# Kernel optimization log

Hardware: AMD Instinct MI355X
Metric: run time of the kernel (lower is better)

Reference implementation:

```python
import jax, jax.numpy as jnp
import numpy as np

B, N, D, H = 4, 4096, 1024, 16
DK = D // H


def setup_inputs() -> dict:
    key = jax.random.key(0)
    ks = jax.random.split(key, 11)
    s = 0.02  # small init scale for weights
    return {
        "query": jax.random.normal(ks[0], (B, N, D), jnp.float32),
        "key": jax.random.normal(ks[1], (B, N, D), jnp.float32),
        "value": jax.random.normal(ks[2], (B, N, D), jnp.float32),
        "Wq": jax.random.normal(ks[3], (D, D), jnp.float32) * s,
        "bq": jax.random.normal(ks[4], (D,), jnp.float32) * s,
        "Wk": jax.random.normal(ks[5], (D, D), jnp.float32) * s,
        "bk": jax.random.normal(ks[6], (D,), jnp.float32) * s,
        "Wv": jax.random.normal(ks[7], (D, D), jnp.float32) * s,
        "bv": jax.random.normal(ks[8], (D,), jnp.float32) * s,
        "Wo": jax.random.normal(ks[9], (D, D), jnp.float32) * s,
        "bo": jax.random.normal(ks[10], (D,), jnp.float32) * s,
    }


def reference(query, key, value, Wq, bq, Wk, bk, Wv, bv, Wo, bo):
    b, n, d = query.shape
    h, dk = H, d // H

    def proj(x, W, bias):
        # torch Linear: y = x @ W.T + b ; then split heads -> [b,h,n,dk]
        y = x @ W.T + bias
        return y.reshape(b, n, h, dk).transpose(0, 2, 1, 3)

    q = proj(query, Wq, bq)
    k = proj(key, Wk, bk)
    v = proj(value, Wv, bv)

    # linear attention (Efficient Attention, arXiv:1812.01243)
    q = jax.nn.softmax(q, axis=-1) * (1.0 / np.sqrt(dk).astype(np.float32))
    k = jax.nn.softmax(k, axis=-2)  # softmax over sequence dim
    ctx = jnp.einsum('bhnd,bhne->bhde', k, v)   # [b,h,dk,dk]
    out = jnp.einsum('bhnd,bhde->bhne', q, ctx)  # [b,h,n,dk]

    out = out.transpose(0, 2, 1, 3).reshape(b, n, d)
    return out @ Wo.T + bo
```

## Files before the change

kernel.cpp:

```cpp
#include <hip/hip_runtime.h>
#include <hip/hip_bf16.h>

#define B_ 4
#define N_ 4096
#define D_ 1024
#define H_ 16

typedef __attribute__((ext_vector_type(4))) float f32x4;
typedef __attribute__((ext_vector_type(8))) short s16x8;

__device__ __forceinline__ ushort f2bf(float f) {
  union { float f; unsigned u; } v; v.f = f;
  unsigned u = v.u;
  return (ushort)((u + 0x7fffu + ((u >> 16) & 1u)) >> 16);
}

__device__ __forceinline__ void gld16(const ushort* g, ushort* lds_base) {
  __builtin_amdgcn_global_load_lds(
      (const __attribute__((address_space(1))) unsigned int*)g,
      (__attribute__((address_space(3))) unsigned int*)lds_base, 16, 0, 0);
}

__device__ __forceinline__ unsigned cvtpk(float lo, float hi) {
  unsigned r;
  asm("v_cvt_pk_bf16_f32 %0, %1, %2" : "=v"(r) : "v"(lo), "v"(hi));
  return r;
}

__global__ void conv_w_kernel(const float* __restrict__ w0, const float* __restrict__ w1,
                              const float* __restrict__ w2, const float* __restrict__ w3,
                              ushort* __restrict__ dst) {
  const int z = blockIdx.z;
  const float* src = z == 0 ? w0 : z == 1 ? w1 : z == 2 ? w2 : w3;
  ushort* d = dst + (long)z * (D_ * D_);
  const long i0 = ((long)blockIdx.x * 256 + threadIdx.x) * 8;
  const long STR = (long)128 * 256 * 8;
#pragma unroll
  for (int u = 0; u < 4; ++u) {
    f32x4 a = *(const f32x4*)(src + i0 + u * STR);
    f32x4 b = *(const f32x4*)(src + i0 + u * STR + 4);
    s16x8 o;
    o[0] = (short)f2bf(a[0]); o[1] = (short)f2bf(a[1]); o[2] = (short)f2bf(a[2]); o[3] = (short)f2bf(a[3]);
    o[4] = (short)f2bf(b[0]); o[5] = (short)f2bf(b[1]); o[6] = (short)f2bf(b[2]); o[7] = (short)f2bf(b[3]);
    *(s16x8*)(d + i0 + u * STR) = o;
  }
}

template <int EPI, bool AFP32>
__global__ __launch_bounds__(256, 2) void gemm_bt_kernel(
    const void* __restrict__ Av, const ushort* __restrict__ Bm,
    void* __restrict__ Cv, const float* __restrict__ bias, float* __restrict__ kpart,
    int MT, int K, long sA, long sB, long sC) {
  __shared__ ushort As[128 * 32];
  __shared__ ushort Bs[128 * 32];
  const int z = blockIdx.z;
  Bm += (long)z * sB;
  const int lin = blockIdx.x;
  const int xcd = lin & 7, idx = lin >> 3;
  const int mpx = MT >> 3;
  const int m0 = (xcd * mpx + (idx >> 3)) * 128;
  const int n0 = (idx & 7) * 128;
  const int N = 1024;
  const int tid = threadIdx.x;
  const int wave = tid >> 6, lane = tid & 63;
  const int fl = lane & 15, fh = lane >> 4;
  const int wm = wave >> 1, wn = wave & 1;
  f32x4 acc[4][4] = {};
  const int rb0 = tid >> 2, kb0 = (tid & 3) * 8;
  const int rb1 = (tid + 256) >> 2, kb1 = ((tid + 256) & 3) * 8;
  ushort* ldsB0 = Bs + wave * 512;
  ushort* ldsB1 = Bs + 2048 + wave * 512;
  ushort* ldsA0 = As + wave * 512;
  ushort* ldsA1 = As + 2048 + wave * 512;

  const float* Af = (const float*)Av;
  const ushort* Ab = (const ushort*)Av + (long)z * sA;
  const float* ap = AFP32 ? (Af + (long)(m0 + (tid >> 3)) * K + (tid & 7) * 4) : nullptr;
  ushort* wp = As + (tid >> 3) * 32 + (tid & 7) * 4;
  f32x4 areg[4];
  if constexpr (AFP32) {
#pragma unroll
    for (int u = 0; u < 4; ++u) areg[u] = *(const f32x4*)(ap + u * 32 * 1024);
  }

  for (int kk = 0; kk < K; kk += 32) {
    __syncthreads();
    gld16(Bm + (long)(n0 + rb0) * K + kk + kb0, ldsB0);
    gld16(Bm + (long)(n0 + rb1) * K + kk + kb1, ldsB1);
    if constexpr (AFP32) {
#pragma unroll
      for (int u = 0; u < 4; ++u) {
        uint2 w;
        w.x = cvtpk(areg[u][0], areg[u][1]);
        w.y = cvtpk(areg[u][2], areg[u][3]);
        *(uint2*)(wp + u * 1024) = w;
      }
      if (kk + 32 < K) {
#pragma unroll
        for (int u = 0; u < 4; ++u)
          areg[u] = *(const f32x4*)(ap + u * 32 * 1024 + kk + 32);
      }
    } else {
      gld16(Ab + (long)(m0 + rb0) * K + kk + kb0, ldsA0);
      gld16(Ab + (long)(m0 + rb1) * K + kk + kb1, ldsA1);
    }
    __syncthreads();
    s16x8 fa[4], fb[4];
#pragma unroll
    for (int i = 0; i < 4; ++i)
      fa[i] = *(const s16x8*)(As + (wm * 64 + i * 16 + fl) * 32 + fh * 8);
#pragma unroll
    for (int j = 0; j < 4; ++j)
      fb[j] = *(const s16x8*)(Bs + (wn * 64 + j * 16 + fl) * 32 + fh * 8);
#pragma unroll
    for (int i = 0; i < 4; ++i)
#pragma unroll
      for (int j = 0; j < 4; ++j)
        acc[i][j] = __builtin_amdgcn_mfma_f32_16x16x32_bf16(fa[i], fb[j], acc[i][j], 0, 0, 0);
  }

  if constexpr (EPI == 0) {
    ushort* C = (ushort*)Cv;
#pragma unroll
    for (int j = 0; j < 4; ++j) {
      int col = n0 + wn * 64 + j * 16 + fl;
#pragma unroll
      for (int i = 0; i < 4; ++i)
#pragma unroll
        for (int r = 0; r < 4; ++r) {
          int row = m0 + wm * 64 + i * 16 + fh * 4 + r;
          C[(long)row * N + col] = f2bf(acc[i][j][r]);
        }
    }
  } else if constexpr (EPI == 1) {
    ushort* C = (ushort*)Cv;
    float bcol[4];
#pragma unroll
    for (int j = 0; j < 4; ++j) bcol[j] = bias[n0 + wn * 64 + j * 16 + fl];
#pragma unroll
    for (int i = 0; i < 4; ++i)
#pragma unroll
      for (int r = 0; r < 4; ++r) {
        float v[4];
#pragma unroll
        for (int j = 0; j < 4; ++j) v[j] = acc[i][j][r] + bcol[j];
        float m = fmaxf(fmaxf(v[0], v[1]), fmaxf(v[2], v[3]));
#pragma unroll
        for (int o = 1; o <= 8; o <<= 1) m = fmaxf(m, __shfl_xor(m, o));
        float e[4], s = 0.f;
#pragma unroll
        for (int j = 0; j < 4; ++j) { e[j] = __expf(v[j] - m); s += e[j]; }
#pragma unroll
        for (int o = 1; o <= 8; o <<= 1) s += __shfl_xor(s, o);
        float sc = 0.125f / s;
        int row = m0 + wm * 64 + i * 16 + fh * 4 + r;
#pragma unroll
        for (int j = 0; j < 4; ++j)
          C[(long)row * N + n0 + wn * 64 + j * 16 + fl] = f2bf(e[j] * sc);
      }
  } else if constexpr (EPI == 2) {
    ushort* C = (ushort*)Cv;
    float csum[4] = {};
#pragma unroll
    for (int j = 0; j < 4; ++j) {
      int col = n0 + wn * 64 + j * 16 + fl;
#pragma unroll
      for (int i = 0; i < 4; ++i)
#pragma unroll
        for (int r = 0; r < 4; ++r) {
          int row = m0 + wm * 64 + i * 16 + fh * 4 + r;
          float e = __expf(acc[i][j][r]);
          csum[j] += e;
          C[(long)row * N + col] = f2bf(e);
        }
    }
#pragma unroll
    for (int j = 0; j < 4; ++j) {
#pragma unroll
      for (int o = 16; o <= 32; o <<= 1) csum[j] += __shfl_xor(csum[j], o);
    }
    if (fh == 0) {
      int b = m0 >> 12;
      int chunk = ((m0 & 4095) >> 7) * 2 + wm;
#pragma unroll
      for (int j = 0; j < 4; ++j)
        kpart[(long)b * 65536 + (long)chunk * 1024 + n0 + wn * 64 + j * 16 + fl] = csum[j];
    }
  } else {
    float* C = (float*)Cv + (long)z * sC;
#pragma unroll
    for (int j = 0; j < 4; ++j) {
      int col = n0 + wn * 64 + j * 16 + fl;
      float bv = bias[col];
#pragma unroll
      for (int i = 0; i < 4; ++i)
#pragma unroll
        for (int r = 0; r < 4; ++r) {
          int row = m0 + wm * 64 + i * 16 + fh * 4 + r;
          C[(long)row * N + col] = acc[i][j][r] + bv;
        }
    }
  }
}

__global__ void ksm2_kernel(const float* __restrict__ kpart, float* __restrict__ colinv) {
  int idx = blockIdx.x * 256 + threadIdx.x;
  int b = idx >> 10, d = idx & 1023;
  float s = 0.f;
  for (int c = 0; c < 64; ++c) s += kpart[(long)b * 65536 + (long)c * 1024 + d];
  colinv[idx] = 1.0f / s;
}

__global__ __launch_bounds__(256, 2) void ctx_partial_kernel(
    const ushort* __restrict__ Ksm, const ushort* __restrict__ Vp, float* __restrict__ part) {
  __shared__ ushort Ks[128 * 64];
  __shared__ ushort Vs[128 * 64];
  const int chunk = blockIdx.x;
  const int bh = blockIdx.y;
  const int b = bh >> 4, h = bh & 15;
  const int tid = threadIdx.x, wave = tid >> 6, lane = tid & 63;
  const int fl = lane & 15, fh = lane >> 4;
  f32x4 acc[4] = {};
  for (int t = 0; t < 4; ++t) {
    const long base = ((long)(b * N_ + chunk * 512 + t * 128)) * D_ + h * 64;
    __syncthreads();
#pragma unroll
    for (int i = 0; i < 4; ++i) {
      int c = i * 256 + tid;
      int r = c >> 3, k8 = (c & 7) * 8;
      ushort* lk = Ks + (long)(i * 256 + wave * 64) * 8;
      ushort* lv = Vs + (long)(i * 256 + wave * 64) * 8;
      gld16(Ksm + base + (long)r * D_ + k8, lk);
      gld16(Vp + base + (long)r * D_ + k8, lv);
    }
    __syncthreads();
#pragma unroll
    for (int s = 0; s < 4; ++s) {
      s16x8 fa;
#pragma unroll
      for (int j = 0; j < 8; ++j)
        fa[j] = (short)Ks[(s * 32 + fh * 8 + j) * 64 + wave * 16 + fl];
#pragma unroll
      for (int jt = 0; jt < 4; ++jt) {
        s16x8 fb;
#pragma unroll
        for (int j = 0; j < 8; ++j)
          fb[j] = (short)Vs[(s * 32 + fh * 8 + j) * 64 + jt * 16 + fl];
        acc[jt] = __builtin_amdgcn_mfma_f32_16x16x32_bf16(fa, fb, acc[jt], 0, 0, 0);
      }
    }
  }
  float* dst = part + ((long)chunk * 64 + bh) * 4096;
#pragma unroll
  for (int jt = 0; jt < 4; ++jt)
#pragma unroll
    for (int r = 0; r < 4; ++r)
      dst[(wave * 16 + fh * 4 + r) * 64 + jt * 16 + fl] = acc[jt][r];
}

__global__ void ctx_reduce_kernel(const float* __restrict__ part, const float* __restrict__ bv,
                                  const float* __restrict__ colinv, ushort* __restrict__ ctxb) {
  int idx = blockIdx.x * 256 + threadIdx.x;
  int e = idx & 63;
  int dk = (idx >> 6) & 63;
  int h = (idx >> 12) & 15;
  int b = idx >> 16;
  float s = 0.f;
#pragma unroll
  for (int c = 0; c < 8; ++c) s += part[(long)c * 262144 + idx];
  ctxb[idx] = f2bf(s * colinv[b * 1024 + h * 64 + dk] + bv[h * 64 + e]);
}

__global__ __launch_bounds__(256, 2) void mb_kernel(
    const ushort* __restrict__ Wob, const ushort* __restrict__ ctxb, ushort* __restrict__ Mb) {
  const int o0 = blockIdx.x * 64, h = blockIdx.y, b = blockIdx.z;
  const int tid = threadIdx.x, wave = tid >> 6, lane = tid & 63;
  const int fl = lane & 15, fh = lane >> 4;
  const ushort* ctxh = ctxb + ((long)(b * 16 + h)) * 4096;
  f32x4 acc[4] = {};
#pragma unroll
  for (int s = 0; s < 2; ++s) {
    s16x8 fa = *(const s16x8*)(Wob + (long)(o0 + wave * 16 + fl) * D_ + h * 64 + s * 32 + fh * 8);
#pragma unroll
    for (int jt = 0; jt < 4; ++jt) {
      s16x8 fb = *(const s16x8*)(ctxh + (long)(jt * 16 + fl) * 64 + s * 32 + fh * 8);
      acc[jt] = __builtin_amdgcn_mfma_f32_16x16x32_bf16(fa, fb, acc[jt], 0, 0, 0);
    }
  }
  ushort* dst = Mb + (long)b * (D_ * D_);
#pragma unroll
  for (int jt = 0; jt < 4; ++jt)
#pragma unroll
    for (int r = 0; r < 4; ++r)
      dst[(long)(o0 + wave * 16 + fh * 4 + r) * D_ + h * 64 + jt * 16 + fl] = f2bf(acc[jt][r]);
}

extern "C" void kernel_launch(void* const* d_in, const int* in_sizes, int n_in,
                              void* d_out, int out_size, void* d_ws, size_t ws_size,
                              hipStream_t stream) {
  const float* q_in = (const float*)d_in[0];
  const float* k_in = (const float*)d_in[1];
  const float* v_in = (const float*)d_in[2];
  const float* Wq = (const float*)d_in[3];
  const float* bq = (const float*)d_in[4];
  const float* Wk = (const float*)d_in[5];
  const float* Wv = (const float*)d_in[7];
  const float* bv = (const float*)d_in[8];
  const float* Wo = (const float*)d_in[9];
  const float* bo = (const float*)d_in[10];

  char* ws = (char*)d_ws;
  ushort* Wb = (ushort*)(ws + 0);
  ushort* Qp = (ushort*)(ws + 8388608);
  ushort* Kp = (ushort*)(ws + 41943040);
  ushort* Vp = (ushort*)(ws + 75497472);
  float* kpart = (float*)(ws + 109051904);
  float* colinv = (float*)(ws + 110100480);
  float* ctxpart = (float*)(ws + 110116864);
  ushort* ctxb = (ushort*)(ws + 118505472);
  ushort* Mb = (ushort*)(ws + 119029760);

  ushort* Wbq = Wb;
  ushort* Wbk = Wb + 1048576;
  ushort* Wbv = Wb + 2097152;
  ushort* Wbo = Wb + 3145728;

  conv_w_kernel<<<dim3(128, 1, 4), 256, 0, stream>>>(Wq, Wk, Wv, Wo, Wb);

  gemm_bt_kernel<1, true><<<dim3(1024, 1, 1), 256, 0, stream>>>(
      q_in, Wbq, Qp, bq, nullptr, 128, 1024, 0, 0, 0);
  gemm_bt_kernel<2, true><<<dim3(1024, 1, 1), 256, 0, stream>>>(
      k_in, Wbk, Kp, nullptr, kpart, 128, 1024, 0, 0, 0);
  gemm_bt_kernel<0, true><<<dim3(1024, 1, 1), 256, 0, stream>>>(
      v_in, Wbv, Vp, nullptr, nullptr, 128, 1024, 0, 0, 0);

  ksm2_kernel<<<16, 256, 0, stream>>>(kpart, colinv);

  ctx_partial_kernel<<<dim3(8, 64), 256, 0, stream>>>(Kp, Vp, ctxpart);
  ctx_reduce_kernel<<<1024, 256, 0, stream>>>(ctxpart, bv, colinv, ctxb);
  mb_kernel<<<dim3(16, 16, 4), 256, 0, stream>>>(Wbo, ctxb, Mb);

  gemm_bt_kernel<3, false><<<dim3(256, 1, 4), 256, 0, stream>>>(
      Qp, Mb, (float*)d_out, bo, nullptr, 32, 1024,
      (long)4096 * 1024, (long)1024 * 1024, (long)4096 * 1024);
}
```

Before: 263.5 us.

## Double-buffer GEMM mainloop with K=64 tiles, swizzled LDS and manual waits

Rewrites the shared GEMM mainloop to use K=64 tiles in double-buffered LDS, with an XOR swizzle on the LDS layout to avoid bank conflicts. fp32 activations are prefetched one tile ahead in registers and converted to bf16 while the MFMAs run on the other buffer. It uses explicit vmcnt/lgkmcnt waits and raw barriers instead of two __syncthreads per step. It also drops the XCD-aware block remapping in favour of a plain 2D grid. In exchange, LDS use quadruples to 64KB per block, which could limit occupancy to two blocks, and the hand-placed waits add correctness risk.

```diff
diff --git a/kernel.cpp b/kernel.cpp
--- a/kernel.cpp
+++ b/kernel.cpp
@@ -8,6 +8,7 @@
 
 typedef __attribute__((ext_vector_type(4))) float f32x4;
 typedef __attribute__((ext_vector_type(8))) short s16x8;
+typedef __attribute__((ext_vector_type(4))) unsigned int u32x4;
 
 __device__ __forceinline__ ushort f2bf(float f) {
   union { float f; unsigned u; } v; v.f = f;
@@ -26,6 +27,11 @@
   asm("v_cvt_pk_bf16_f32 %0, %1, %2" : "=v"(r) : "v"(lo), "v"(hi));
   return r;
 }
+
+#define WAITVM(N) asm volatile("s_waitcnt vmcnt(" #N ")" ::: "memory")
+#define LGKM0 asm volatile("s_waitcnt lgkmcnt(0)" ::: "memory")
+#define SBAR __builtin_amdgcn_sched_barrier(0)
+#define BARRIER __builtin_amdgcn_s_barrier()
 
 __global__ void conv_w_kernel(const float* __restrict__ w0, const float* __restrict__ w1,
                               const float* __restrict__ w2, const float* __restrict__ w3,
@@ -47,77 +53,113 @@
 }
 
 template <int EPI, bool AFP32>
-__global__ __launch_bounds__(256, 2) void gemm_bt_kernel(
+__device__ __forceinline__ void gemm_body(
     const void* __restrict__ Av, const ushort* __restrict__ Bm,
     void* __restrict__ Cv, const float* __restrict__ bias, float* __restrict__ kpart,
-    int MT, int K, long sA, long sB, long sC) {
-  __shared__ ushort As[128 * 32];
-  __shared__ ushort Bs[128 * 32];
-  const int z = blockIdx.z;
-  Bm += (long)z * sB;
-  const int lin = blockIdx.x;
-  const int xcd = lin & 7, idx = lin >> 3;
-  const int mpx = MT >> 3;
-  const int m0 = (xcd * mpx + (idx >> 3)) * 128;
-  const int n0 = (idx & 7) * 128;
+    int m0, int n0) {
+  __shared__ ushort As[16384];
+  __shared__ ushort Bs[16384];
   const int N = 1024;
   const int tid = threadIdx.x;
-  const int wave = tid >> 6, lane = tid & 63;
+  const int lane = tid & 63, wave = tid >> 6;
   const int fl = lane & 15, fh = lane >> 4;
   const int wm = wave >> 1, wn = wave & 1;
   f32x4 acc[4][4] = {};
-  const int rb0 = tid >> 2, kb0 = (tid & 3) * 8;
-  const int rb1 = (tid + 256) >> 2, kb1 = ((tid + 256) & 3) * 8;
-  ushort* ldsB0 = Bs + wave * 512;
-  ushort* ldsB1 = Bs + 2048 + wave * 512;
-  ushort* ldsA0 = As + wave * 512;
-  ushort* ldsA1 = As + 2048 + wave * 512;
-
-  const float* Af = (const float*)Av;
-  const ushort* Ab = (const ushort*)Av + (long)z * sA;
-  const float* ap = AFP32 ? (Af + (long)(m0 + (tid >> 3)) * K + (tid & 7) * 4) : nullptr;
-  ushort* wp = As + (tid >> 3) * 32 + (tid & 7) * 4;
-  f32x4 areg[4];
+
+  const int r0 = tid >> 3;
+  const int scol = ((tid & 7) ^ (r0 & 7)) * 8;
+  const ushort* Bsrc = Bm + (long)(n0 + r0) * 1024 + scol;
+  const ushort* Ab = (const ushort*)Av;
+  const ushort* Asrc = AFP32 ? nullptr : (Ab + (long)(m0 + r0) * 1024 + scol);
+
+  const int ar = tid >> 1, ch = tid & 1;
+  const float* apA = AFP32 ? ((const float*)Av + (long)(m0 + ar) * 1024 + ch * 32) : nullptr;
+  int awo[4];
+#pragma unroll
+  for (int w = 0; w < 4; ++w) awo[w] = ar * 64 + (((ch * 4 + w) ^ (ar & 7)) * 8);
+
+  f32x4 pa0, pa1, pa2, pa3, pa4, pa5, pa6, pa7;
+  f32x4 pb0, pb1, pb2, pb3, pb4, pb5, pb6, pb7;
+
+#define GLD_B(T, CUR) do { \
+    _Pragma("unroll") for (int i = 0; i < 4; ++i) \
+      gld16(Bsrc + (T) * 64 + i * 32768, Bs + (CUR) * 8192 + tid * 8 + i * 2048); } while (0)
+#define GLD_A(T, CUR) do { \
+    _Pragma("unroll") for (int i = 0; i < 4; ++i) \
+      gld16(Asrc + (T) * 64 + i * 32768, As + (CUR) * 8192 + tid * 8 + i * 2048); } while (0)
+#define PLOAD(T, S) do { \
+    S##0 = *(const f32x4*)(apA + (T) * 64);      S##1 = *(const f32x4*)(apA + (T) * 64 + 4); \
+    S##2 = *(const f32x4*)(apA + (T) * 64 + 8);  S##3 = *(const f32x4*)(apA + (T) * 64 + 12); \
+    S##4 = *(const f32x4*)(apA + (T) * 64 + 16); S##5 = *(const f32x4*)(apA + (T) * 64 + 20); \
+    S##6 = *(const f32x4*)(apA + (T) * 64 + 24); S##7 = *(const f32x4*)(apA + (T) * 64 + 28); } while (0)
+#define CVT_WRITE(S, CUR) do { \
+    u32x4 _w; \
+    _w[0] = cvtpk(S##0[0], S##0[1]); _w[1] = cvtpk(S##0[2], S##0[3]); \
+    _w[2] = cvtpk(S##1[0], S##1[1]); _w[3] = cvtpk(S##1[2], S##1[3]); \
+    *(u32x4*)(As + (CUR) * 8192 + awo[0]) = _w; \
+    _w[0] = cvtpk(S##2[0], S##2[1]); _w[1] = cvtpk(S##2[2], S##2[3]); \
+    _w[2] = cvtpk(S##3[0], S##3[1]); _w[3] = cvtpk(S##3[2], S##3[3]); \
+    *(u32x4*)(As + (CUR) * 8192 + awo[1]) = _w; \
+    _w[0] = cvtpk(S##4[0], S##4[1]); _w[1] = cvtpk(S##4[2], S##4[3]); \
+    _w[2] = cvtpk(S##5[0], S##5[1]); _w[3] = cvtpk(S##5[2], S##5[3]); \
+    *(u32x4*)(As + (CUR) * 8192 + awo[2]) = _w; \
+    _w[0] = cvtpk(S##6[0], S##6[1]); _w[1] = cvtpk(S##6[2], S##6[3]); \
+    _w[2] = cvtpk(S##7[0], S##7[1]); _w[3] = cvtpk(S##7[2], S##7[3]); \
+    *(u32x4*)(As + (CUR) * 8192 + awo[3]) = _w; } while (0)
+#define MFMA_STEP(CUR) do { \
+    _Pragma("unroll") for (int h2 = 0; h2 < 2; ++h2) { \
+      s16x8 fb[4]; \
+      _Pragma("unroll") for (int j = 0; j < 4; ++j) \
+        fb[j] = *(const s16x8*)(Bs + (CUR) * 8192 + (wn * 64 + j * 16 + fl) * 64 + \
+                                (((h2 * 4 + fh) ^ (fl & 7)) * 8)); \
+      _Pragma("unroll") for (int i = 0; i < 4; ++i) { \
+        s16x8 fa = *(const s16x8*)(As + (CUR) * 8192 + (wm * 64 + i * 16 + fl) * 64 + \
+                                   (((h2 * 4 + fh) ^ (fl & 7)) * 8)); \
+        _Pragma("unroll") for (int j = 0; j < 4; ++j) \
+          acc[i][j] = __builtin_amdgcn_mfma_f32_16x16x32_bf16(fa, fb[j], acc[i][j], 0, 0, 0); \
+      } } } while (0)
+
   if constexpr (AFP32) {
-#pragma unroll
-    for (int u = 0; u < 4; ++u) areg[u] = *(const f32x4*)(ap + u * 32 * 1024);
+    PLOAD(0, pa);
+    CVT_WRITE(pa, 0);
+    GLD_B(0, 0);
+    PLOAD(1, pb);
+    WAITVM(8); LGKM0; BARRIER; SBAR;
+#pragma unroll 1
+    for (int t = 0; t < 14; t += 2) {
+      CVT_WRITE(pb, 1);
+      GLD_B(t + 1, 1);
+      PLOAD(t + 2, pa);
+      MFMA_STEP(0);
+      WAITVM(8); LGKM0; BARRIER; SBAR;
+      CVT_WRITE(pa, 0);
+      GLD_B(t + 2, 0);
+      PLOAD(t + 3, pb);
+      MFMA_STEP(1);
+      WAITVM(8); LGKM0; BARRIER; SBAR;
+    }
+    CVT_WRITE(pb, 1);
+    GLD_B(15, 1);
+    MFMA_STEP(0);
+    WAITVM(0); LGKM0; BARRIER; SBAR;
+    MFMA_STEP(1);
+  } else {
+    GLD_A(0, 0); GLD_B(0, 0);
+    WAITVM(0); BARRIER; SBAR;
+#pragma unroll 1
+    for (int t = 0; t < 15; ++t) {
+      GLD_A(t + 1, (t + 1) & 1);
+      GLD_B(t + 1, (t + 1) & 1);
+      MFMA_STEP(t & 1);
+      WAITVM(0); BARRIER; SBAR;
+    }
+    MFMA_STEP(1);
   }
-
-  for (int kk = 0; kk < K; kk += 32) {
-    __syncthreads();
-    gld16(Bm + (long)(n0 + rb0) * K + kk + kb0, ldsB0);
-    gld16(Bm + (long)(n0 + rb1) * K + kk + kb1, ldsB1);
-    if constexpr (AFP32) {
-#pragma unroll
-      for (int u = 0; u < 4; ++u) {
-        uint2 w;
-        w.x = cvtpk(areg[u][0], areg[u][1]);
-        w.y = cvtpk(areg[u][2], areg[u][3]);
-        *(uint2*)(wp + u * 1024) = w;
-      }
-      if (kk + 32 < K) {
-#pragma unroll
-        for (int u = 0; u < 4; ++u)
-          areg[u] = *(const f32x4*)(ap + u * 32 * 1024 + kk + 32);
-      }
-    } else {
-      gld16(Ab + (long)(m0 + rb0) * K + kk + kb0, ldsA0);
-      gld16(Ab + (long)(m0 + rb1) * K + kk + kb1, ldsA1);
-    }
-    __syncthreads();
-    s16x8 fa[4], fb[4];
-#pragma unroll
-    for (int i = 0; i < 4; ++i)
-      fa[i] = *(const s16x8*)(As + (wm * 64 + i * 16 + fl) * 32 + fh * 8);
-#pragma unroll
-    for (int j = 0; j < 4; ++j)
-      fb[j] = *(const s16x8*)(Bs + (wn * 64 + j * 16 + fl) * 32 + fh * 8);
-#pragma unroll
-    for (int i = 0; i < 4; ++i)
-#pragma unroll
-      for (int j = 0; j < 4; ++j)
-        acc[i][j] = __builtin_amdgcn_mfma_f32_16x16x32_bf16(fa[i], fb[j], acc[i][j], 0, 0, 0);
-  }
+#undef GLD_B
+#undef GLD_A
+#undef PLOAD
+#undef CVT_WRITE
+#undef MFMA_STEP
 
   if constexpr (EPI == 0) {
     ushort* C = (ushort*)Cv;
@@ -187,7 +229,7 @@
         kpart[(long)b * 65536 + (long)chunk * 1024 + n0 + wn * 64 + j * 16 + fl] = csum[j];
     }
   } else {
-    float* C = (float*)Cv + (long)z * sC;
+    float* C = (float*)Cv;
 #pragma unroll
     for (int j = 0; j < 4; ++j) {
       int col = n0 + wn * 64 + j * 16 + fl;
@@ -201,6 +243,33 @@
         }
     }
   }
+}
+
+__global__ __launch_bounds__(256, 2) void gemm_q(const float* __restrict__ A,
+                                                 const ushort* __restrict__ Bm,
+                                                 ushort* __restrict__ C,
+                                                 const float* __restrict__ bias) {
+  gemm_body<1, true>(A, Bm, C, bias, nullptr, blockIdx.x * 128, blockIdx.y * 128);
+}
+__global__ __launch_bounds__(256, 2) void gemm_k(const float* __restrict__ A,
+                                                 const ushort* __restrict__ Bm,
+                                                 ushort* __restrict__ C,
+                                                 float* __restrict__ kpart) {
+  gemm_body<2, true>(A, Bm, C, nullptr, kpart, blockIdx.x * 128, blockIdx.y * 128);
+}
+__global__ __launch_bounds__(256, 2) void gemm_v(const float* __restrict__ A,
+                                                 const ushort* __restrict__ Bm,
+                                                 ushort* __restrict__ C) {
+  gemm_body<0, true>(A, Bm, C, nullptr, nullptr, blockIdx.x * 128, blockIdx.y * 128);
+}
+__global__ __launch_bounds__(256, 2) void gemm_o(const ushort* __restrict__ A,
+                                                 const ushort* __restrict__ Bm,
+                                                 float* __restrict__ C,
+                                                 const float* __restrict__ bias) {
+  const int z = blockIdx.z;
+  gemm_body<3, false>(A + (long)z * 4096 * 1024, Bm + (long)z * 1024 * 1024,
+                      C + (long)z * 4096 * 1024, bias, nullptr,
+                      blockIdx.x * 128, blockIdx.y * 128);
 }
 
 __global__ void ksm2_kernel(const float* __restrict__ kpart, float* __restrict__ colinv) {
@@ -327,12 +396,9 @@
 
   conv_w_kernel<<<dim3(128, 1, 4), 256, 0, stream>>>(Wq, Wk, Wv, Wo, Wb);
 
-  gemm_bt_kernel<1, true><<<dim3(1024, 1, 1), 256, 0, stream>>>(
-      q_in, Wbq, Qp, bq, nullptr, 128, 1024, 0, 0, 0);
-  gemm_bt_kernel<2, true><<<dim3(1024, 1, 1), 256, 0, stream>>>(
-      k_in, Wbk, Kp, nullptr, kpart, 128, 1024, 0, 0, 0);
-  gemm_bt_kernel<0, true><<<dim3(1024, 1, 1), 256, 0, stream>>>(
-      v_in, Wbv, Vp, nullptr, nullptr, 128, 1024, 0, 0, 0);
+  gemm_q<<<dim3(128, 8), 256, 0, stream>>>(q_in, Wbq, Qp, bq);
+  gemm_k<<<dim3(128, 8), 256, 0, stream>>>(k_in, Wbk, Kp, kpart);
+  gemm_v<<<dim3(128, 8), 256, 0, stream>>>(v_in, Wbv, Vp);
 
   ksm2_kernel<<<16, 256, 0, stream>>>(kpart, colinv);
 
@@ -340,7 +406,5 @@
   ctx_reduce_kernel<<<1024, 256, 0, stream>>>(ctxpart, bv, colinv, ctxb);
   mb_kernel<<<dim3(16, 16, 4), 256, 0, stream>>>(Wbo, ctxb, Mb);
 
-  gemm_bt_kernel<3, false><<<dim3(256, 1, 4), 256, 0, stream>>>(
-      Qp, Mb, (float*)d_out, bo, nullptr, 32, 1024,
-      (long)4096 * 1024, (long)1024 * 1024, (long)4096 * 1024);
-}
+  gemm_o<<<dim3(32, 8, 4), 256, 0, stream>>>(Qp, Mb, (float*)d_out, bo);
+}
```

Result: slower. 373.2 us (+41.6%).
